# Performance work log

Measured on AMD Instinct MI355X. Metric: run time of the kernel, lower is better.

Reference implementation:

```python
import jax, jax.numpy as jnp
import numpy as np

WS = 7       # window_size
SHIFT = 3    # shift
NH = 4       # n_heads


def _rel_index(ws: int) -> np.ndarray:
    # matches torch.cartesian_prod(arange(ws), arange(ws)) ordering (second index fastest)
    coords = np.stack(np.meshgrid(np.arange(ws), np.arange(ws), indexing='ij'), -1).reshape(-1, 2)
    d = coords[:, None, :] - coords[None, :, :]
    idx = (d[..., 0] + ws - 1) * (2 * ws - 1) + d[..., 1] + ws - 1
    return idx.reshape(-1).astype(np.int32)  # [ws*ws*ws*ws]


def _ln(x, g, b, eps=1e-5):
    m = x.mean(-1, keepdims=True)
    v = ((x - m) ** 2).mean(-1, keepdims=True)
    return (x - m) / jnp.sqrt(v + eps) * g + b


def setup_inputs() -> dict:
    key = jax.random.key(0)
    ks = jax.random.split(key, 14)
    B, H, W, C = 64, 56, 56, 128
    hidden = int(C * 4.0)
    s = 0.02
    return {
        'x': jax.random.normal(ks[0], (B, H, W, C), jnp.float32),
        'norm1_g': jnp.ones((C,), jnp.float32),
        'norm1_b': jnp.zeros((C,), jnp.float32),
        'qkv_w': jax.random.normal(ks[1], (3 * C, C), jnp.float32) * s,
        'qkv_b': jnp.zeros((3 * C,), jnp.float32),
        'out_w': jax.random.normal(ks[2], (C, C), jnp.float32) * s,
        'out_b': jnp.zeros((C,), jnp.float32),
        'pe_table': jax.random.normal(ks[3], (NH, (2 * WS - 1) ** 2), jnp.float32) * s,
        'norm2_g': jnp.ones((C,), jnp.float32),
        'norm2_b': jnp.zeros((C,), jnp.float32),
        'mlp_w1': jax.random.normal(ks[4], (hidden, C), jnp.float32) * s,
        'mlp_b1': jnp.zeros((hidden,), jnp.float32),
        'mlp_w2': jax.random.normal(ks[5], (C, hidden), jnp.float32) * s,
        'mlp_b2': jnp.zeros((C,), jnp.float32),
    }


def reference(x, norm1_g, norm1_b, qkv_w, qkv_b, out_w, out_b, pe_table,
              norm2_g, norm2_b, mlp_w1, mlp_b1, mlp_w2, mlp_b2):
    B, H, W, C = x.shape
    nH, nW = H // WS, W // WS
    L = WS * WS
    hd = C // NH

    h = _ln(x, norm1_g, norm1_b)
    h = jnp.roll(h, (SHIFT, SHIFT), (1, 2))  # shifted windows (no inverse roll in source)

    # window partition: [B,H,W,C] -> [B*nH*nW, L, C]
    h = h.reshape(B, nH, WS, nW, WS, C).transpose(0, 1, 3, 2, 4, 5).reshape(B * nH * nW, L, C)

    qkv = h @ qkv_w.T + qkv_b  # [N, L, 3C]
    q, k, v = jnp.split(qkv, 3, axis=-1)
    to_heads = lambda t: t.reshape(-1, L, NH, hd).transpose(0, 2, 1, 3)  # [N,h,L,hd]
    q, k, v = to_heads(q), to_heads(k), to_heads(v)

    idx = jnp.asarray(_rel_index(WS))
    bias = pe_table[:, idx].reshape(NH, L, L)  # gathered relative position bias

    scores = jnp.einsum('nhqd,nhkd->nhqk', q, k) / jnp.sqrt(jnp.float32(hd)) + bias[None]
    attn = jax.nn.softmax(scores, axis=-1)
    o = jnp.einsum('nhqk,nhkd->nhqd', attn, v).transpose(0, 2, 1, 3).reshape(-1, L, C)
    o = o @ out_w.T + out_b

    # window unpartition: [B*nH*nW, L, C] -> [B,H,W,C]
    o = o.reshape(B, nH, nW, WS, WS, C).transpose(0, 1, 3, 2, 4, 5).reshape(B, H, W, C)

    h2 = _ln(o, norm2_g, norm2_b)
    y = jax.nn.gelu(h2 @ mlp_w1.T + mlp_b1, approximate=False) @ mlp_w2.T + mlp_b2
    return y
```

## Files before the change

kernel.cpp:

```cpp
#include <hip/hip_runtime.h>
#include <hip/hip_bf16.h>


#define NWIN 4096
#define HB 7440
#define KOFF 2568
#define VOFF 5136

typedef __attribute__((ext_vector_type(8))) short s8v;
typedef __attribute__((ext_vector_type(4))) float f4v;

__device__ __forceinline__ void split2(float v, unsigned short& h, unsigned short& l) {
    unsigned int b = __float_as_uint(v);
    h = (unsigned short)(b >> 16);
    float hf = __uint_as_float(b & 0xFFFF0000u);
    __hip_bfloat16 lo = __float2bfloat16(v - hf);
    l = *reinterpret_cast<unsigned short*>(&lo);
}
__device__ __forceinline__ unsigned short bfr(float v) {
    __hip_bfloat16 h = __float2bfloat16(v);
    return *reinterpret_cast<unsigned short*>(&h);
}

__global__ __launch_bounds__(256) void presplit_kernel(
    const float* __restrict__ qkvw, const float* __restrict__ outw,
    const float* __restrict__ w1, const float* __restrict__ w2,
    unsigned short* __restrict__ P)
{
    int i = blockIdx.x * 256 + threadIdx.x;
    if (i >= 196608) return;
    if (i < 49152) {
        float v = qkvw[i];
        if (i < 16384) v *= 0.17677669529663687f;
        unsigned short h, l; split2(v, h, l);
        P[i] = h; P[49152 + i] = l;
    } else if (i < 65536) {
        int j = i - 49152;
        P[98304 + j] = bfr(outw[j]);
    } else if (i < 131072) {
        int j = i - 65536;
        P[114688 + j] = bfr(w1[j]);
    } else {
        int j = i - 131072;
        P[180224 + j] = bfr(w2[j]);
    }
}

__global__ __launch_bounds__(256) void ln_qkv(
    const float* __restrict__ x,
    const float* __restrict__ g, const float* __restrict__ bta,
    const unsigned short* __restrict__ W,
    const float* __restrict__ bias,
    unsigned short* __restrict__ OutQK, unsigned short* __restrict__ OutV,
    int M, int tbase)
{
    __shared__ __align__(16) unsigned short Ah[64 * 40];
    __shared__ __align__(16) unsigned short Al[64 * 40];
    __shared__ __align__(16) unsigned short Wh[64 * 40];
    __shared__ __align__(16) unsigned short Wl[64 * 40];
    int tid = threadIdx.x;
    int m0 = blockIdx.y * 64, n0 = blockIdx.x * 64;
    int sr = tid >> 2, sq = (tid & 3) * 8;
    int ar = m0 + sr; if (ar >= M) ar = M - 1;
    int t = tbase + ar;
    int n = t / 49, l = t - n * 49;
    int b = n >> 6, wh_ = (n >> 3) & 7, ww = n & 7;
    int i = l / 7, j = l - i * 7;
    int sh = (wh_ * 7 + i + 53) % 56, sw = (ww * 7 + j + 53) % 56;
    const float* ip = x + (size_t)((b * 56 + sh) * 56 + sw) * 128;

    float v[4][8];
    float s = 0.f, q2 = 0.f;
    #pragma unroll
    for (int kc = 0; kc < 4; ++kc) {
        float4 a = *reinterpret_cast<const float4*>(ip + kc * 32 + sq);
        float4 c = *reinterpret_cast<const float4*>(ip + kc * 32 + sq + 4);
        v[kc][0] = a.x; v[kc][1] = a.y; v[kc][2] = a.z; v[kc][3] = a.w;
        v[kc][4] = c.x; v[kc][5] = c.y; v[kc][6] = c.z; v[kc][7] = c.w;
        #pragma unroll
        for (int e = 0; e < 8; ++e) { s += v[kc][e]; q2 += v[kc][e] * v[kc][e]; }
    }
    s  += __shfl_xor(s, 1);  s  += __shfl_xor(s, 2);
    q2 += __shfl_xor(q2, 1); q2 += __shfl_xor(q2, 2);
    float mean = s * (1.0f / 128.0f);
    float var  = q2 * (1.0f / 128.0f) - mean * mean;
    float rstd = rsqrtf(var + 1e-5f);
    unsigned short ah[4][8], al[4][8];
    #pragma unroll
    for (int kc = 0; kc < 4; ++kc)
        #pragma unroll
        for (int e = 0; e < 8; ++e) {
            int c = kc * 32 + sq + e;
            float r = (v[kc][e] - mean) * rstd * g[c] + bta[c];
            split2(r, ah[kc][e], al[kc][e]);
        }

    int wv = tid >> 6, ln = tid & 63;
    int wm = wv & 1, wn = wv >> 1;
    int fm = ln & 15, fq = ln >> 4;
    const unsigned short* Whg = W;
    const unsigned short* Wlg = W + 49152;
    size_t wrow = (size_t)(n0 + sr) * 128 + sq;
    int so = sr * 40 + sq;
    s8v rwh = *reinterpret_cast<const s8v*>(Whg + wrow);
    s8v rwl = *reinterpret_cast<const s8v*>(Wlg + wrow);

    f4v acc[2][2] = {};
    #pragma unroll
    for (int kc = 0; kc < 4; ++kc) {
        *reinterpret_cast<s8v*>(&Ah[so]) = *reinterpret_cast<const s8v*>(ah[kc]);
        *reinterpret_cast<s8v*>(&Al[so]) = *reinterpret_cast<const s8v*>(al[kc]);
        *reinterpret_cast<s8v*>(&Wh[so]) = rwh;
        *reinterpret_cast<s8v*>(&Wl[so]) = rwl;
        __syncthreads();
        if (kc < 3) {
            rwh = *reinterpret_cast<const s8v*>(Whg + wrow + (kc + 1) * 32);
            rwl = *reinterpret_cast<const s8v*>(Wlg + wrow + (kc + 1) * 32);
        }
        s8v fah[2], fal[2], fbh[2], fbl[2];
        #pragma unroll
        for (int tt = 0; tt < 2; ++tt) {
            int ao = (wm * 32 + tt * 16 + fm) * 40 + fq * 8;
            fah[tt] = *reinterpret_cast<const s8v*>(&Ah[ao]);
            fal[tt] = *reinterpret_cast<const s8v*>(&Al[ao]);
            int bo = (wn * 32 + tt * 16 + fm) * 40 + fq * 8;
            fbh[tt] = *reinterpret_cast<const s8v*>(&Wh[bo]);
            fbl[tt] = *reinterpret_cast<const s8v*>(&Wl[bo]);
        }
        #pragma unroll
        for (int tm = 0; tm < 2; ++tm)
            #pragma unroll
            for (int tn = 0; tn < 2; ++tn) {
                acc[tm][tn] = __builtin_amdgcn_mfma_f32_16x16x32_bf16(fah[tm], fbh[tn], acc[tm][tn], 0, 0, 0);
                acc[tm][tn] = __builtin_amdgcn_mfma_f32_16x16x32_bf16(fah[tm], fbl[tn], acc[tm][tn], 0, 0, 0);
                acc[tm][tn] = __builtin_amdgcn_mfma_f32_16x16x32_bf16(fal[tm], fbh[tn], acc[tm][tn], 0, 0, 0);
            }
        __syncthreads();
    }

    #pragma unroll
    for (int tm = 0; tm < 2; ++tm)
        #pragma unroll
        for (int tn = 0; tn < 2; ++tn) {
            int col = n0 + wn * 32 + tn * 16 + fm;
            float bv = bias[col];
            if (col < 128) bv *= 0.17677669529663687f;
            #pragma unroll
            for (int r = 0; r < 4; ++r) {
                int m = m0 + wm * 32 + tm * 16 + fq * 4 + r;
                if (m >= M) continue;
                float vv = acc[tm][tn][r] + bv;
                if (col < 256) {
                    OutQK[(size_t)m * 256 + col] = bfr(vv);
                } else {
                    int dd = col - 256, hh = dd >> 5, d = dd & 31;
                    int win = m / 49, l2 = m - win * 49;
                    int kp = (l2 & 15) * 4 + (l2 >> 4);
                    OutV[((size_t)win * 128 + hh * 32 + d) * 64 + kp] = bfr(vv);
                }
            }
        }
}

__global__ void bias_tab_kernel(const float* __restrict__ pe, float* __restrict__ tab) {
    int t = threadIdx.x;
    int h = t >> 6, ln = t & 63;
    int g = ln >> 4, c = ln & 15;
    for (int mt = 0; mt < 4; ++mt)
        for (int nt = 0; nt < 4; ++nt)
            for (int r = 0; r < 4; ++r) {
                int l1 = mt * 16 + g * 4 + r, l2 = nt * 16 + c;
                float b = 0.f;
                if (l1 < 49 && l2 < 49) {
                    int i1 = l1 / 7, j1 = l1 % 7, i2 = l2 / 7, j2 = l2 % 7;
                    b = pe[h * 169 + (i1 - i2 + 6) * 13 + (j1 - j2 + 6)];
                }
                tab[((h * 64 + ln) * 16 + mt * 4 + nt) * 4 + r] = b;
            }
}

__global__ __launch_bounds__(256) void attn_mfma(
    const unsigned short* __restrict__ qk,
    const unsigned short* __restrict__ vt,
    const float* __restrict__ btab,
    unsigned short* __restrict__ oH)
{
    __shared__ __align__(16) unsigned short lds[4 * HB];
    int tid = threadIdx.x;
    int win = blockIdx.x;
    const unsigned short* srcqk = qk + (size_t)win * 49 * 256;
    const unsigned short* srcv  = vt + (size_t)win * 8192;

    for (int idx = tid; idx < 1568; idx += 256) {
        int l2 = idx >> 5, c8 = idx & 31;
        int d8 = c8 * 8;
        s8v v8 = *reinterpret_cast<const s8v*>(srcqk + (size_t)l2 * 256 + d8);
        int sec = d8 >> 7, dd = d8 & 127, hh = dd >> 5, kk = dd & 31;
        *reinterpret_cast<s8v*>(&lds[hh * HB + (sec ? KOFF : 0) + l2 * 40 + kk]) = v8;
    }
    for (int idx = tid; idx < 1024; idx += 256) {
        int row = idx >> 3, j = idx & 7;
        s8v v8 = *reinterpret_cast<const s8v*>(srcv + (size_t)row * 64 + j * 8);
        int hh = row >> 5, d = row & 31;
        *reinterpret_cast<s8v*>(&lds[hh * HB + VOFF + d * 72 + j * 8]) = v8;
    }
    __syncthreads();
    for (int i = tid; i < 1920; i += 256) {
        int hh = i / 480, rem = i % 480, d = rem / 15, j = rem % 15;
        lds[hh * HB + VOFF + d * 72 + (j + 1) * 4 + 3] = 0;
    }
    __syncthreads();

    int h = tid >> 6, ln = tid & 63;
    int fm = ln & 15, fq = ln >> 4;
    int base = h * HB;

    s8v Qf[4], Kf[4];
    #pragma unroll
    for (int t = 0; t < 4; ++t) {
        Qf[t] = *reinterpret_cast<const s8v*>(&lds[base + (t * 16 + fm) * 40 + fq * 8]);
        Kf[t] = *reinterpret_cast<const s8v*>(&lds[base + KOFF + (t * 16 + fm) * 40 + fq * 8]);
    }
    f4v S[4][4] = {};
    #pragma unroll
    for (int mt = 0; mt < 4; ++mt)
        #pragma unroll
        for (int nt = 0; nt < 4; ++nt)
            S[mt][nt] = __builtin_amdgcn_mfma_f32_16x16x32_bf16(Qf[mt], Kf[nt], S[mt][nt], 0, 0, 0);
    #pragma unroll
    for (int mt = 0; mt < 4; ++mt)
        #pragma unroll
        for (int nt = 0; nt < 4; ++nt)
            S[mt][nt] += *reinterpret_cast<const f4v*>(&btab[((h * 64 + ln) * 16 + mt * 4 + nt) * 4]);

    float rcp[16];
    #pragma unroll
    for (int mt = 0; mt < 4; ++mt) {
        #pragma unroll
        for (int r = 0; r < 4; ++r) {
            float v0 = S[mt][0][r], v1 = S[mt][1][r], v2 = S[mt][2][r], v3 = S[mt][3][r];
            if (fm != 0) v3 = -1e30f;
            float mx = fmaxf(fmaxf(v0, v1), fmaxf(v2, v3));
            #pragma unroll
            for (int off = 1; off < 16; off <<= 1) mx = fmaxf(mx, __shfl_xor(mx, off));
            float e0 = __expf(v0 - mx), e1 = __expf(v1 - mx);
            float e2 = __expf(v2 - mx), e3 = __expf(v3 - mx);
            float sm = e0 + e1 + e2 + e3;
            #pragma unroll
            for (int off = 1; off < 16; off <<= 1) sm += __shfl_xor(sm, off);
            rcp[mt * 4 + r] = 1.0f / sm;
            int row = mt * 16 + fq * 4 + r;
            ushort4 pk = { bfr(e0), bfr(e1), bfr(e2), bfr(e3) };
            *reinterpret_cast<ushort4*>(&lds[base + row * 72 + fm * 4]) = pk;
        }
    }

    f4v O[4][2] = {};
    #pragma unroll
    for (int kt = 0; kt < 2; ++kt) {
        s8v Pf[4], Vf[2];
        #pragma unroll
        for (int mt = 0; mt < 4; ++mt)
            Pf[mt] = *reinterpret_cast<const s8v*>(&lds[base + (mt * 16 + fm) * 72 + kt * 32 + fq * 8]);
        #pragma unroll
        for (int nt = 0; nt < 2; ++nt)
            Vf[nt] = *reinterpret_cast<const s8v*>(&lds[base + VOFF + (nt * 16 + fm) * 72 + kt * 32 + fq * 8]);
        #pragma unroll
        for (int mt = 0; mt < 4; ++mt)
            #pragma unroll
            for (int nt = 0; nt < 2; ++nt)
                O[mt][nt] = __builtin_amdgcn_mfma_f32_16x16x32_bf16(Pf[mt], Vf[nt], O[mt][nt], 0, 0, 0);
    }

    size_t ob = (size_t)win * 49 * 128 + h * 32;
    #pragma unroll
    for (int mt = 0; mt < 4; ++mt)
        #pragma unroll
        for (int r = 0; r < 4; ++r) {
            int row = mt * 16 + fq * 4 + r;
            if (row < 49) {
                float sc = rcp[mt * 4 + r];
                #pragma unroll
                for (int nt = 0; nt < 2; ++nt)
                    oH[ob + (size_t)row * 128 + nt * 16 + fm] = bfr(O[mt][nt][r] * sc);
            }
        }
}

__global__ __launch_bounds__(256) void proj_ln(
    const unsigned short* __restrict__ Ag,
    const unsigned short* __restrict__ Wg,
    const float* __restrict__ bias,
    const float* __restrict__ g, const float* __restrict__ bta,
    unsigned short* __restrict__ Out, int M)
{
    __shared__ __align__(16) unsigned short As[64 * 132];
    __shared__ __align__(16) unsigned short Ws[128 * 40];
    __shared__ float red[2][2][64];
    int tid = threadIdx.x;
    int m0 = blockIdx.x * 64;
    for (int c = tid; c < 1024; c += 256) {
        int row = c >> 4, c8 = (c & 15) * 8;
        int ar = m0 + row; if (ar >= M) ar = M - 1;
        *reinterpret_cast<s8v*>(&As[row * 132 + c8]) =
            *reinterpret_cast<const s8v*>(Ag + (size_t)ar * 128 + c8);
    }
    int w0r = tid >> 2, w0c = (tid & 3) * 8;
    int w1r = 64 + w0r;
    s8v rw0 = *reinterpret_cast<const s8v*>(Wg + (size_t)w0r * 128 + w0c);
    s8v rw1 = *reinterpret_cast<const s8v*>(Wg + (size_t)w1r * 128 + w0c);

    int wv = tid >> 6, ln = tid & 63;
    int wm = wv & 1, wn = wv >> 1;
    int fm = ln & 15, fq = ln >> 4;
    f4v acc[2][4] = {};
    for (int kc = 0; kc < 4; ++kc) {
        *reinterpret_cast<s8v*>(&Ws[w0r * 40 + w0c]) = rw0;
        *reinterpret_cast<s8v*>(&Ws[w1r * 40 + w0c]) = rw1;
        __syncthreads();
        if (kc < 3) {
            rw0 = *reinterpret_cast<const s8v*>(Wg + (size_t)w0r * 128 + (kc + 1) * 32 + w0c);
            rw1 = *reinterpret_cast<const s8v*>(Wg + (size_t)w1r * 128 + (kc + 1) * 32 + w0c);
        }
        s8v fa[2], fb[4];
        #pragma unroll
        for (int t = 0; t < 2; ++t)
            fa[t] = *reinterpret_cast<const s8v*>(&As[(wm * 32 + t * 16 + fm) * 132 + kc * 32 + fq * 8]);
        #pragma unroll
        for (int t = 0; t < 4; ++t)
            fb[t] = *reinterpret_cast<const s8v*>(&Ws[(wn * 64 + t * 16 + fm) * 40 + fq * 8]);
        #pragma unroll
        for (int tm = 0; tm < 2; ++tm)
            #pragma unroll
            for (int tn = 0; tn < 4; ++tn)
                acc[tm][tn] = __builtin_amdgcn_mfma_f32_16x16x32_bf16(fa[tm], fb[tn], acc[tm][tn], 0, 0, 0);
        __syncthreads();
    }
    float sumv[2][4], sqv[2][4];
    #pragma unroll
    for (int tm = 0; tm < 2; ++tm)
        #pragma unroll
        for (int r = 0; r < 4; ++r) {
            float s = 0.f, q = 0.f;
            #pragma unroll
            for (int tn = 0; tn < 4; ++tn) {
                float v = acc[tm][tn][r] + bias[wn * 64 + tn * 16 + fm];
                acc[tm][tn][r] = v;
                s += v; q += v * v;
            }
            #pragma unroll
            for (int off = 1; off < 16; off <<= 1) { s += __shfl_xor(s, off); q += __shfl_xor(q, off); }
            sumv[tm][r] = s; sqv[tm][r] = q;
        }
    if (fm == 0) {
        #pragma unroll
        for (int tm = 0; tm < 2; ++tm)
            #pragma unroll
            for (int r = 0; r < 4; ++r) {
                int row = wm * 32 + tm * 16 + fq * 4 + r;
                red[wn][0][row] = sumv[tm][r];
                red[wn][1][row] = sqv[tm][r];
            }
    }
    __syncthreads();
    #pragma unroll
    for (int tm = 0; tm < 2; ++tm)
        #pragma unroll
        for (int r = 0; r < 4; ++r) {
            int row = wm * 32 + tm * 16 + fq * 4 + r;
            int m = m0 + row;
            float s = red[0][0][row] + red[1][0][row];
            float q = red[0][1][row] + red[1][1][row];
            float mean = s * (1.0f / 128.0f);
            float var  = q * (1.0f / 128.0f) - mean * mean;
            float rstd = rsqrtf(var + 1e-5f);
            if (m < M) {
                #pragma unroll
                for (int tn = 0; tn < 4; ++tn) {
                    int nn = wn * 64 + tn * 16 + fm;
                    float o = (acc[tm][tn][r] - mean) * rstd * g[nn] + bta[nn];
                    Out[(size_t)m * 128 + nn] = bfr(o);
                }
            }
        }
}

__global__ __launch_bounds__(256) void gemm_w(
    const unsigned short* __restrict__ A, const unsigned short* __restrict__ W,
    const float* __restrict__ bias,
    float* __restrict__ OutF, unsigned short* __restrict__ OutH,
    int M, int N, int K, int mode, int tbase)
{
    __shared__ __align__(16) unsigned short As[64 * 40];
    __shared__ __align__(16) unsigned short Ws[128 * 40];
    int tid = threadIdx.x;
    int wv = tid >> 6, ln = tid & 63;
    int wm = wv & 1, wn = wv >> 1;
    int fm = ln & 15, fq = ln >> 4;
    int m0 = blockIdx.y * 64, n0 = blockIdx.x * 128;
    int sr = tid >> 2, sk = (tid & 3) * 8;
    int arow = m0 + sr; if (arow >= M) arow = M - 1;
    const unsigned short* pA  = A + (size_t)arow * K + sk;
    const unsigned short* pW0 = W + (size_t)(n0 + sr) * K + sk;
    const unsigned short* pW1 = W + (size_t)(n0 + 64 + sr) * K + sk;
    int so = sr * 40 + sk;

    f4v acc[2][4] = {};
    s8v ra, rw0, rw1;
    #define LOADK(k0) do { \
        ra  = *reinterpret_cast<const s8v*>(pA  + (k0)); \
        rw0 = *reinterpret_cast<const s8v*>(pW0 + (k0)); \
        rw1 = *reinterpret_cast<const s8v*>(pW1 + (k0)); } while (0)
    LOADK(0);
    for (int k0 = 0; k0 < K; k0 += 32) {
        *reinterpret_cast<s8v*>(&As[so]) = ra;
        *reinterpret_cast<s8v*>(&Ws[so]) = rw0;
        *reinterpret_cast<s8v*>(&Ws[2560 + so]) = rw1;
        __syncthreads();
        if (k0 + 32 < K) LOADK(k0 + 32);
        s8v fa[2], fb[4];
        #pragma unroll
        for (int t = 0; t < 2; ++t)
            fa[t] = *reinterpret_cast<const s8v*>(&As[(wm * 32 + t * 16 + fm) * 40 + fq * 8]);
        #pragma unroll
        for (int t = 0; t < 4; ++t)
            fb[t] = *reinterpret_cast<const s8v*>(&Ws[(wn * 64 + t * 16 + fm) * 40 + fq * 8]);
        #pragma unroll
        for (int tm = 0; tm < 2; ++tm)
            #pragma unroll
            for (int tn = 0; tn < 4; ++tn)
                acc[tm][tn] = __builtin_amdgcn_mfma_f32_16x16x32_bf16(fa[tm], fb[tn], acc[tm][tn], 0, 0, 0);
        __syncthreads();
    }
    #undef LOADK

    #pragma unroll
    for (int tm = 0; tm < 2; ++tm)
        #pragma unroll
        for (int tn = 0; tn < 4; ++tn) {
            int col = n0 + wn * 64 + tn * 16 + fm;
            float bv = bias[col];
            #pragma unroll
            for (int r = 0; r < 4; ++r) {
                int m = m0 + wm * 32 + tm * 16 + fq * 4 + r;
                if (m >= M) continue;
                float v = acc[tm][tn][r] + bv;
                if (mode == 1) {
                    v = 0.5f * v * (1.0f + erff(v * 0.70710678118654752f));
                    OutH[(size_t)m * N + col] = bfr(v);
                } else {
                    int t = tbase + m;
                    int n = t / 49, l = t - n * 49;
                    int b = n >> 6, wh_ = (n >> 3) & 7, ww = n & 7;
                    int i = l / 7, jj = l - i * 7;
                    size_t orow = (size_t)((b * 56 + wh_ * 7 + i) * 56 + ww * 7 + jj);
                    OutF[orow * N + col] = v;
                }
            }
        }
}

extern "C" void kernel_launch(void* const* d_in, const int* in_sizes, int n_in,
                              void* d_out, int out_size, void* d_ws, size_t ws_size,
                              hipStream_t stream) {
    const float* x    = (const float*)d_in[0];
    const float* n1g  = (const float*)d_in[1];
    const float* n1b  = (const float*)d_in[2];
    const float* qkvw = (const float*)d_in[3];
    const float* qkvb = (const float*)d_in[4];
    const float* outw = (const float*)d_in[5];
    const float* outb = (const float*)d_in[6];
    const float* pe   = (const float*)d_in[7];
    const float* n2g  = (const float*)d_in[8];
    const float* n2b  = (const float*)d_in[9];
    const float* w1   = (const float*)d_in[10];
    const float* b1   = (const float*)d_in[11];
    const float* w2   = (const float*)d_in[12];
    const float* b2   = (const float*)d_in[13];
    float* y = (float*)d_out;

    size_t wpc = NWIN;
    while (wpc > 8 && 557056 + wpc * 116736ULL > ws_size) wpc >>= 1;
    const int nchunks = (int)(NWIN / wpc);
    const size_t rows = wpc * 49;

    char* ws = (char*)d_ws;
    float* btab = (float*)ws;
    unsigned short* wpl = (unsigned short*)(ws + 65536);
    unsigned short* bufQK = (unsigned short*)(ws + 557056);
    unsigned short* bufV  = bufQK + rows * 256;
    unsigned short* bufO  = bufV + wpc * 8192;
    unsigned short* bufL  = bufO + rows * 128;
    unsigned short* bufH  = bufL + rows * 128;
    const int gy = (int)((rows + 63) / 64);

    presplit_kernel<<<768, 256, 0, stream>>>(qkvw, outw, w1, w2, wpl);
    bias_tab_kernel<<<1, 256, 0, stream>>>(pe, btab);

    for (int c = 0; c < nchunks; ++c) {
        int tbase = (int)(c * wpc * 49);
        ln_qkv<<<dim3(6, gy), 256, 0, stream>>>(
            x, n1g, n1b, wpl, qkvb, bufQK, bufV, (int)rows, tbase);
        attn_mfma<<<(int)wpc, 256, 0, stream>>>(bufQK, bufV, btab, bufO);
        proj_ln<<<gy, 256, 0, stream>>>(bufO, wpl + 98304, outb, n2g, n2b, bufL, (int)rows);
        gemm_w<<<dim3(4, gy), 256, 0, stream>>>(
            bufL, wpl + 114688, b1, nullptr, bufH, (int)rows, 512, 128, 1, 0);
        gemm_w<<<dim3(1, gy), 256, 0, stream>>>(
            bufH, wpl + 180224, b2, y, nullptr, (int)rows, 128, 512, 3, tbase);
    }
}
```

Measured before the change: 709.3 us.

## Fuse MLP up-projection, GELU and down-projection into one kernel

Replaces the two separate MLP GEMM launches with a single kernel that keeps each 64-row tile's hidden activations in shared memory. It loops over 64-wide hidden slices, computing GELU(xW1+b1) into LDS and accumulating the W2 product in registers, so the bf16 hidden tensor is no longer written to or read from global memory. It also drops the hidden buffer from the workspace sizing and caps the chunk at 1024 windows, which means more chunk iterations and more launches. Each block now re-streams all of W1 and W2, and the second GEMM uses only one block per row tile, which lowers parallelism.

```diff
diff --git a/kernel.cpp b/kernel.cpp
--- a/kernel.cpp
+++ b/kernel.cpp
@@ -385,77 +385,117 @@
         }
 }
 
-__global__ __launch_bounds__(256) void gemm_w(
-    const unsigned short* __restrict__ A, const unsigned short* __restrict__ W,
-    const float* __restrict__ bias,
-    float* __restrict__ OutF, unsigned short* __restrict__ OutH,
-    int M, int N, int K, int mode, int tbase)
+__global__ __launch_bounds__(256) void mlp_fused(
+    const unsigned short* __restrict__ Ag,
+    const unsigned short* __restrict__ W1g,
+    const unsigned short* __restrict__ W2g,
+    const float* __restrict__ b1, const float* __restrict__ b2,
+    float* __restrict__ y, int M, int tbase)
 {
-    __shared__ __align__(16) unsigned short As[64 * 40];
-    __shared__ __align__(16) unsigned short Ws[128 * 40];
+    __shared__ __align__(16) unsigned short W1s[64 * 136];
+    __shared__ __align__(16) unsigned short W2s[128 * 72];
+    __shared__ __align__(16) unsigned short Hs[64 * 72];
     int tid = threadIdx.x;
+    int m0 = blockIdx.x * 64;
     int wv = tid >> 6, ln = tid & 63;
     int wm = wv & 1, wn = wv >> 1;
     int fm = ln & 15, fq = ln >> 4;
-    int m0 = blockIdx.y * 64, n0 = blockIdx.x * 128;
-    int sr = tid >> 2, sk = (tid & 3) * 8;
-    int arow = m0 + sr; if (arow >= M) arow = M - 1;
-    const unsigned short* pA  = A + (size_t)arow * K + sk;
-    const unsigned short* pW0 = W + (size_t)(n0 + sr) * K + sk;
-    const unsigned short* pW1 = W + (size_t)(n0 + 64 + sr) * K + sk;
-    int so = sr * 40 + sk;
-
-    f4v acc[2][4] = {};
-    s8v ra, rw0, rw1;
-    #define LOADK(k0) do { \
-        ra  = *reinterpret_cast<const s8v*>(pA  + (k0)); \
-        rw0 = *reinterpret_cast<const s8v*>(pW0 + (k0)); \
-        rw1 = *reinterpret_cast<const s8v*>(pW1 + (k0)); } while (0)
-    LOADK(0);
-    for (int k0 = 0; k0 < K; k0 += 32) {
-        *reinterpret_cast<s8v*>(&As[so]) = ra;
-        *reinterpret_cast<s8v*>(&Ws[so]) = rw0;
-        *reinterpret_cast<s8v*>(&Ws[2560 + so]) = rw1;
-        __syncthreads();
-        if (k0 + 32 < K) LOADK(k0 + 32);
-        s8v fa[2], fb[4];
-        #pragma unroll
-        for (int t = 0; t < 2; ++t)
-            fa[t] = *reinterpret_cast<const s8v*>(&As[(wm * 32 + t * 16 + fm) * 40 + fq * 8]);
-        #pragma unroll
-        for (int t = 0; t < 4; ++t)
-            fb[t] = *reinterpret_cast<const s8v*>(&Ws[(wn * 64 + t * 16 + fm) * 40 + fq * 8]);
+
+    s8v fa[2][4];
+    #pragma unroll
+    for (int t = 0; t < 2; ++t) {
+        int ar = m0 + wm * 32 + t * 16 + fm; if (ar >= M) ar = M - 1;
+        #pragma unroll
+        for (int kk = 0; kk < 4; ++kk)
+            fa[t][kk] = *reinterpret_cast<const s8v*>(Ag + (size_t)ar * 128 + kk * 32 + fq * 8);
+    }
+
+    int w1row = tid >> 2, w1q = (tid & 3) * 32;
+    int w2row = tid >> 1, w2q = (tid & 1) * 32;
+    s8v rw1[4], rw2[4];
+    #pragma unroll
+    for (int e = 0; e < 4; ++e) {
+        rw1[e] = *reinterpret_cast<const s8v*>(W1g + (size_t)w1row * 128 + w1q + e * 8);
+        rw2[e] = *reinterpret_cast<const s8v*>(W2g + (size_t)w2row * 512 + w2q + e * 8);
+    }
+
+    f4v acc2[2][4] = {};
+    for (int j = 0; j < 8; ++j) {
+        #pragma unroll
+        for (int e = 0; e < 4; ++e) {
+            *reinterpret_cast<s8v*>(&W1s[w1row * 136 + w1q + e * 8]) = rw1[e];
+            *reinterpret_cast<s8v*>(&W2s[w2row * 72  + w2q + e * 8]) = rw2[e];
+        }
+        __syncthreads();
+        if (j < 7) {
+            #pragma unroll
+            for (int e = 0; e < 4; ++e) {
+                rw1[e] = *reinterpret_cast<const s8v*>(W1g + (size_t)((j + 1) * 64 + w1row) * 128 + w1q + e * 8);
+                rw2[e] = *reinterpret_cast<const s8v*>(W2g + (size_t)w2row * 512 + (j + 1) * 64 + w2q + e * 8);
+            }
+        }
+        f4v acc1[2][2] = {};
+        #pragma unroll
+        for (int kk = 0; kk < 4; ++kk) {
+            s8v fb[2];
+            #pragma unroll
+            for (int t = 0; t < 2; ++t)
+                fb[t] = *reinterpret_cast<const s8v*>(&W1s[(wn * 32 + t * 16 + fm) * 136 + kk * 32 + fq * 8]);
+            #pragma unroll
+            for (int tm = 0; tm < 2; ++tm)
+                #pragma unroll
+                for (int tn = 0; tn < 2; ++tn)
+                    acc1[tm][tn] = __builtin_amdgcn_mfma_f32_16x16x32_bf16(fa[tm][kk], fb[tn], acc1[tm][tn], 0, 0, 0);
+        }
         #pragma unroll
         for (int tm = 0; tm < 2; ++tm)
             #pragma unroll
+            for (int tn = 0; tn < 2; ++tn) {
+                int nl = wn * 32 + tn * 16 + fm;
+                float bv = b1[j * 64 + nl];
+                #pragma unroll
+                for (int r = 0; r < 4; ++r) {
+                    float v = acc1[tm][tn][r] + bv;
+                    v = 0.5f * v * (1.0f + erff(v * 0.70710678118654752f));
+                    int mrow = wm * 32 + tm * 16 + fq * 4 + r;
+                    Hs[mrow * 72 + nl] = bfr(v);
+                }
+            }
+        __syncthreads();
+        #pragma unroll
+        for (int kt = 0; kt < 2; ++kt) {
+            s8v hf[2], wf[4];
+            #pragma unroll
+            for (int t = 0; t < 2; ++t)
+                hf[t] = *reinterpret_cast<const s8v*>(&Hs[(wm * 32 + t * 16 + fm) * 72 + kt * 32 + fq * 8]);
+            #pragma unroll
             for (int tn = 0; tn < 4; ++tn)
-                acc[tm][tn] = __builtin_amdgcn_mfma_f32_16x16x32_bf16(fa[tm], fb[tn], acc[tm][tn], 0, 0, 0);
-        __syncthreads();
-    }
-    #undef LOADK
-
+                wf[tn] = *reinterpret_cast<const s8v*>(&W2s[(wn * 64 + tn * 16 + fm) * 72 + kt * 32 + fq * 8]);
+            #pragma unroll
+            for (int tm = 0; tm < 2; ++tm)
+                #pragma unroll
+                for (int tn = 0; tn < 4; ++tn)
+                    acc2[tm][tn] = __builtin_amdgcn_mfma_f32_16x16x32_bf16(hf[tm], wf[tn], acc2[tm][tn], 0, 0, 0);
+        }
+        __syncthreads();
+    }
     #pragma unroll
     for (int tm = 0; tm < 2; ++tm)
         #pragma unroll
         for (int tn = 0; tn < 4; ++tn) {
-            int col = n0 + wn * 64 + tn * 16 + fm;
-            float bv = bias[col];
+            int col = wn * 64 + tn * 16 + fm;
+            float bv = b2[col];
             #pragma unroll
             for (int r = 0; r < 4; ++r) {
                 int m = m0 + wm * 32 + tm * 16 + fq * 4 + r;
                 if (m >= M) continue;
-                float v = acc[tm][tn][r] + bv;
-                if (mode == 1) {
-                    v = 0.5f * v * (1.0f + erff(v * 0.70710678118654752f));
-                    OutH[(size_t)m * N + col] = bfr(v);
-                } else {
-                    int t = tbase + m;
-                    int n = t / 49, l = t - n * 49;
-                    int b = n >> 6, wh_ = (n >> 3) & 7, ww = n & 7;
-                    int i = l / 7, jj = l - i * 7;
-                    size_t orow = (size_t)((b * 56 + wh_ * 7 + i) * 56 + ww * 7 + jj);
-                    OutF[orow * N + col] = v;
-                }
+                float v = acc2[tm][tn][r] + bv;
+                int t = tbase + m;
+                int n = t / 49, l = t - n * 49;
+                int b = n >> 6, wh_ = (n >> 3) & 7, ww = n & 7;
+                int i = l / 7, jj = l - i * 7;
+                size_t orow = (size_t)((b * 56 + wh_ * 7 + i) * 56 + ww * 7 + jj);
+                y[orow * 128 + col] = v;
             }
         }
 }
@@ -480,7 +520,8 @@
     float* y = (float*)d_out;
 
     size_t wpc = NWIN;
-    while (wpc > 8 && 557056 + wpc * 116736ULL > ws_size) wpc >>= 1;
+    while (wpc > 8 && 557056 + wpc * 66560ULL > ws_size) wpc >>= 1;
+    if (wpc > 1024) wpc = 1024;
     const int nchunks = (int)(NWIN / wpc);
     const size_t rows = wpc * 49;
 
@@ -491,7 +532,6 @@
     unsigned short* bufV  = bufQK + rows * 256;
     unsigned short* bufO  = bufV + wpc * 8192;
     unsigned short* bufL  = bufO + rows * 128;
-    unsigned short* bufH  = bufL + rows * 128;
     const int gy = (int)((rows + 63) / 64);
 
     presplit_kernel<<<768, 256, 0, stream>>>(qkvw, outw, w1, w2, wpl);
@@ -503,9 +543,7 @@
             x, n1g, n1b, wpl, qkvb, bufQK, bufV, (int)rows, tbase);
         attn_mfma<<<(int)wpc, 256, 0, stream>>>(bufQK, bufV, btab, bufO);
         proj_ln<<<gy, 256, 0, stream>>>(bufO, wpl + 98304, outb, n2g, n2b, bufL, (int)rows);
-        gemm_w<<<dim3(4, gy), 256, 0, stream>>>(
-            bufL, wpl + 114688, b1, nullptr, bufH, (int)rows, 512, 128, 1, 0);
-        gemm_w<<<dim3(1, gy), 256, 0, stream>>>(
-            bufH, wpl + 180224, b2, y, nullptr, (int)rows, 128, 512, 3, tbase);
-    }
-}
+        mlp_fused<<<gy, 256, 0, stream>>>(
+            bufL, wpl + 114688, wpl + 180224, b1, b2, y, (int)rows, tbase);
+    }
+}
```

Measured after the change: 772.9 us. 9.0% more time.
